# Optimization experiments

Measured on AMD Instinct MI355X. Metric: run time of the kernel, lower is better.

The kernel has to match this reference:

```python
import jax, jax.numpy as jnp
import numpy as np

B, T, I, H = 4096, 256, 6, 64


def _gru_layer(x, W_ih, W_hh, b_ih, b_hh):
    # x: [B,T,Din]; W_ih: [3H,Din]; W_hh: [3H,H]
    xg = jnp.einsum('btd,gd->btg', x, W_ih) + b_ih  # [B,T,3H] input projections
    xg = jnp.transpose(xg, (1, 0, 2))               # [T,B,3H] for scan
    h0 = jnp.zeros((x.shape[0], H), dtype=x.dtype)

    def step(h, xg_t):
        hg = h @ W_hh.T + b_hh                      # [B,3H]
        xr, xz, xn = jnp.split(xg_t, 3, axis=-1)
        hr, hz, hn = jnp.split(hg, 3, axis=-1)
        r = jax.nn.sigmoid(xr + hr)
        z = jax.nn.sigmoid(xz + hz)
        n = jnp.tanh(xn + r * hn)
        h_new = (1.0 - z) * n + z * h
        return h_new, h_new

    _, hs = jax.lax.scan(step, h0, xg)              # hs: [T,B,H]
    return jnp.transpose(hs, (1, 0, 2))             # [B,T,H]


def setup_inputs() -> dict:
    key = jax.random.key(0)
    ks = jax.random.split(key, 11)
    s_i0 = 1.0 / np.sqrt(H)
    u = lambda k, shape: jax.random.uniform(k, shape, jnp.float32, -s_i0, s_i0)
    return {
        'x': jax.random.normal(ks[0], (B, T, I), dtype=jnp.float32),
        'W_ih0': u(ks[1], (3 * H, I)),
        'W_hh0': u(ks[2], (3 * H, H)),
        'b_ih0': u(ks[3], (3 * H,)),
        'b_hh0': u(ks[4], (3 * H,)),
        'W_ih1': u(ks[5], (3 * H, H)),
        'W_hh1': u(ks[6], (3 * H, H)),
        'b_ih1': u(ks[7], (3 * H,)),
        'b_hh1': u(ks[8], (3 * H,)),
        'W_fc': u(ks[9], (1, H)),
        'b_fc': u(ks[10], (1,)),
    }


def reference(x, W_ih0, W_hh0, b_ih0, b_hh0, W_ih1, W_hh1, b_ih1, b_hh1, W_fc, b_fc):
    h1 = _gru_layer(x, W_ih0, W_hh0, b_ih0, b_hh0)   # [B,T,H]
    h2 = _gru_layer(h1, W_ih1, W_hh1, b_ih1, b_hh1)  # [B,T,H]
    last = h2[:, -1, :]                              # [B,H] (dropout is identity in eval)
    out = last @ W_fc.T + b_fc                       # [B,1]
    return out[:, 0]                                 # squeeze(-1) -> [B]
```

## Files before the change

### kernel.cpp

```cpp
#include <hip/hip_runtime.h>
#include <stdint.h>

#define TT 256
#define II 6
#define HH 64
#define MB 16

typedef __attribute__((ext_vector_type(8))) _Float16 half8;
typedef __attribute__((ext_vector_type(4))) float f32x4;

#define K_LOG2E  1.44269504f
#define K_2LOG2E 2.88539008f

static __device__ __forceinline__ uint32_t pkh(float a, float b){
    uint16_t ha = __builtin_bit_cast(uint16_t, (_Float16)a);
    uint16_t hb = __builtin_bit_cast(uint16_t, (_Float16)b);
    return (uint32_t)ha | ((uint32_t)hb << 16);
}
static __device__ __forceinline__ half8 mkh8(uint32_t a, uint32_t b, uint32_t c, uint32_t d){
    union { uint32_t u[4]; half8 v; } x;
    x.u[0]=a; x.u[1]=b; x.u[2]=c; x.u[3]=d;
    return x.v;
}
static __device__ __forceinline__ half8 ldq(const uint32_t* p){
    union { uint4 q; half8 v; } x;
    x.q = *(const uint4*)p;
    return x.v;
}

#define MF(C, A, B) C = __builtin_amdgcn_mfma_f32_16x16x32_f16(A, B, C, 0, 0, 0)

static __device__ __forceinline__ uint2 gates(const f32x4& Cr, const f32x4& Cz,
                                              const f32x4& Cxn, const f32x4& Chn,
                                              f32x4& hp)
{
    float hn[4];
    #pragma unroll
    for (int q = 0; q < 4; ++q){
        float er = __builtin_amdgcn_exp2f(-Cr[q]);
        float ez = __builtin_amdgcn_exp2f(-Cz[q]);
        float pa = 1.0f + er, pb = 1.0f + ez;
        float u  = __builtin_amdgcn_rcpf(pa * pb);
        float rg = u * pb;
        float zg = u * pa;
        float v  = Cxn[q] + rg * Chn[q];
        float e  = __builtin_amdgcn_exp2f(-v);
        float ng = (1.0f - e) * __builtin_amdgcn_rcpf(1.0f + e);
        float h2 = ng + zg * (hp[q] - ng);
        hp[q] = h2;
        hn[q] = h2;
    }
    return make_uint2(pkh(hn[0], hn[1]), pkh(hn[2], hn[3]));
}

__global__ __launch_bounds__(512, 2)
void gru2_v6(const float* __restrict__ x,
             const float* __restrict__ Wih0, const float* __restrict__ Whh0,
             const float* __restrict__ bih0, const float* __restrict__ bhh0,
             const float* __restrict__ Wih1, const float* __restrict__ Whh1,
             const float* __restrict__ bih1, const float* __restrict__ bhh1,
             const float* __restrict__ Wfc,  const float* __restrict__ bfc,
             float* __restrict__ out)
{
    __shared__ uint2    xtA[TT][16];
    __shared__ uint32_t xtB[TT][16];
    __shared__ uint32_t h0buf[2][16][36];
    __shared__ uint32_t h1buf[2][16][36];
    __shared__ float    fcpart[256];

    const int tid  = threadIdx.x;
    const int lane = tid & 63;
    const int wg   = tid >> 6;
    const int isL1 = (wg >= 4);
    const int w    = wg & 3;
    const int c    = lane >> 4;
    const int r16  = lane & 15;
    const int b0   = blockIdx.x * MB;

    for (int e = tid; e < TT * 16; e += 512){
        const int t = e & 255, b = e >> 8;
        const int bi_ = (b + t) & 15;
        const float* xp = x + ((size_t)(b0 + b) * TT + t) * II;
        float2 a  = *(const float2*)(xp + 0);
        float2 bb = *(const float2*)(xp + 2);
        float2 cc = *(const float2*)(xp + 4);
        xtA[t][bi_] = make_uint2(pkh(a.x, a.y), pkh(bb.x, bb.y));
        xtB[t][bi_] = pkh(cc.x, cc.y);
    }
    for (int i = tid; i < 2 * 16 * 36; i += 512){
        (&h0buf[0][0][0])[i] = 0u;
        (&h1buf[0][0][0])[i] = 0u;
    }

    const float gsc[3] = { K_LOG2E, K_LOG2E, K_2LOG2E };
    half8 AW[6][2];
    {
        const float* M0 = isL1 ? Wih1 : Whh0;
        #pragma unroll
        for (int m = 0; m < 6; ++m){
            if (m >= 3 && !isL1) continue;
            const float* Wb = (m < 3) ? M0 : Whh1;
            const float s = gsc[m % 3];
            const float* rowp = Wb + (size_t)((m % 3) * 64 + w * 16 + r16) * HH;
            #pragma unroll
            for (int cw = 0; cw < 2; ++cw){
                const float* pp = rowp + cw * 32 + c * 8;
                AW[m][cw] = mkh8(pkh(s*pp[0], s*pp[1]), pkh(s*pp[2], s*pp[3]),
                                 pkh(s*pp[4], s*pp[5]), pkh(s*pp[6], s*pp[7]));
            }
        }
    }

    half8 Ax[3];
    #pragma unroll
    for (int g = 0; g < 3; ++g){
        if (c == 0){
            const float s = gsc[g];
            const float* rowp = Wih0 + (size_t)(g * 64 + w * 16 + r16) * II;
            Ax[g] = mkh8(pkh(s*rowp[0], s*rowp[1]), pkh(s*rowp[2], s*rowp[3]),
                         pkh(s*rowp[4], s*rowp[5]), 0u);
        } else {
            Ax[g] = mkh8(0u, 0u, 0u, 0u);
        }
    }

    const float* bi = isL1 ? bih1 : bih0;
    const float* bh = isL1 ? bhh1 : bhh0;
    const int rq0 = w * 16 + c * 4;
    f32x4 Br, Bz, Bxn, Bhn;
    #pragma unroll
    for (int q = 0; q < 4; ++q){
        Br[q]  = K_LOG2E  * (bi[      rq0 + q] + bh[      rq0 + q]);
        Bz[q]  = K_LOG2E  * (bi[ 64 + rq0 + q] + bh[ 64 + rq0 + q]);
        Bxn[q] = K_2LOG2E *  bi[128 + rq0 + q];
        Bhn[q] = K_2LOG2E *  bh[128 + rq0 + q];
    }

    f32x4 hp = {0.f, 0.f, 0.f, 0.f};

    const uint32_t* rd0p[2] = { &h0buf[0][r16][4*c], &h0buf[1][r16][4*c] };
    const uint32_t* rd1p[2] = { &h1buf[0][r16][4*c], &h1buf[1][r16][4*c] };
    uint2* wr0p[2] = { (uint2*)&h0buf[0][r16][8*w + 2*c], (uint2*)&h0buf[1][r16][8*w + 2*c] };
    uint2* wr1p[2] = { (uint2*)&h1buf[0][r16][8*w + 2*c], (uint2*)&h1buf[1][r16][8*w + 2*c] };

    __syncthreads();

#define TICK(P, D0, D1, TK) do {                                               \
    if (!isL1) { if (D0) {                                                     \
        const int xi = ((r16 + (TK)) & 15);                                    \
        uint2 xa = xtA[(TK)][xi];                                              \
        uint32_t xb = xtB[(TK)][xi];                                           \
        half8 XB = mkh8(xa.x, xa.y, xb, 0u);                                   \
        f32x4 Cr = Br, Cz = Bz, Cxn = Bxn, Chn = Bhn;                          \
        __builtin_amdgcn_s_setprio(1);                                         \
        MF(Cr,  Ax[0], XB);  MF(Cz,  Ax[1], XB);  MF(Cxn, Ax[2], XB);          \
        { half8 HB = ldq(rd0p[P]);                                             \
          MF(Cr, AW[0][0], HB); MF(Cz, AW[1][0], HB); MF(Chn, AW[2][0], HB); } \
        { half8 HB = ldq(rd0p[P] + 16);                                        \
          MF(Cr, AW[0][1], HB); MF(Cz, AW[1][1], HB); MF(Chn, AW[2][1], HB); } \
        __builtin_amdgcn_s_setprio(0);                                         \
        uint2 d = gates(Cr, Cz, Cxn, Chn, hp);                                 \
        *wr0p[(P) ^ 1] = d;                                                    \
    } } else { if (D1) {                                                       \
        f32x4 Cr = Br, Cz = Bz, Cxn = Bxn, Chn = Bhn;                          \
        __builtin_amdgcn_s_setprio(1);                                         \
        { half8 HB = ldq(rd0p[P]);                                             \
          MF(Cr, AW[0][0], HB); MF(Cz, AW[1][0], HB); MF(Cxn, AW[2][0], HB); } \
        { half8 HB = ldq(rd0p[P] + 16);                                        \
          MF(Cr, AW[0][1], HB); MF(Cz, AW[1][1], HB); MF(Cxn, AW[2][1], HB); } \
        { half8 HB = ldq(rd1p[P]);                                             \
          MF(Cr, AW[3][0], HB); MF(Cz, AW[4][0], HB); MF(Chn, AW[5][0], HB); } \
        { half8 HB = ldq(rd1p[P] + 16);                                        \
          MF(Cr, AW[3][1], HB); MF(Cz, AW[4][1], HB); MF(Chn, AW[5][1], HB); } \
        __builtin_amdgcn_s_setprio(0);                                         \
        uint2 d = gates(Cr, Cz, Cxn, Chn, hp);                                 \
        *wr1p[(P) ^ 1] = d;                                                    \
    } }                                                                        \
} while (0)

    TICK(0, true, false, 0);
    __syncthreads();
    #pragma unroll 1
    for (int tk = 1; tk < 255; tk += 2){
        TICK(1, true, true, tk);
        __syncthreads();
        TICK(0, true, true, tk + 1);
        __syncthreads();
    }
    TICK(1, true, true, 255);
    __syncthreads();
    TICK(0, false, true, 256);

#undef TICK

    if (isL1){
        float4 wf = *(const float4*)(Wfc + w * 16 + c * 4);
        fcpart[(w * 4 + c) * 16 + r16] =
            hp[0] * wf.x + hp[1] * wf.y + hp[2] * wf.z + hp[3] * wf.w;
    }
    __syncthreads();
    if (tid < MB){
        float s = bfc[0];
        #pragma unroll
        for (int u = 0; u < 16; ++u) s += fcpart[u * 16 + tid];
        out[b0 + tid] = s;
    }
}

extern "C" void kernel_launch(void* const* d_in, const int* in_sizes, int n_in,
                              void* d_out, int out_size, void* d_ws, size_t ws_size,
                              hipStream_t stream)
{
    const float* x    = (const float*)d_in[0];
    const float* Wih0 = (const float*)d_in[1];
    const float* Whh0 = (const float*)d_in[2];
    const float* bih0 = (const float*)d_in[3];
    const float* bhh0 = (const float*)d_in[4];
    const float* Wih1 = (const float*)d_in[5];
    const float* Whh1 = (const float*)d_in[6];
    const float* bih1 = (const float*)d_in[7];
    const float* bhh1 = (const float*)d_in[8];
    const float* Wfc  = (const float*)d_in[9];
    const float* bfc  = (const float*)d_in[10];
    float* out = (float*)d_out;

    dim3 grid(4096 / MB), block(512);
    gru2_v6<<<grid, block, 0, stream>>>(x, Wih0, Whh0, bih0, bhh0,
                                        Wih1, Whh1, bih1, bhh1,
                                        Wfc, bfc, out);
}
```

Baseline: 143.1 us.

## Stream x from global per step and precompute next input projection off critical path

```diff
diff --git a/kernel.cpp b/kernel.cpp
--- a/kernel.cpp
+++ b/kernel.cpp
@@ -16,6 +16,9 @@
     uint16_t ha = __builtin_bit_cast(uint16_t, (_Float16)a);
     uint16_t hb = __builtin_bit_cast(uint16_t, (_Float16)b);
     return (uint32_t)ha | ((uint32_t)hb << 16);
+}
+static __device__ __forceinline__ uint32_t pkrtz(float a, float b){
+    return __builtin_bit_cast(uint32_t, __builtin_amdgcn_cvt_pkrtz(a, b));
 }
 static __device__ __forceinline__ half8 mkh8(uint32_t a, uint32_t b, uint32_t c, uint32_t d){
     union { uint32_t u[4]; half8 v; } x;
@@ -47,14 +50,13 @@
         float e  = __builtin_amdgcn_exp2f(-v);
         float ng = (1.0f - e) * __builtin_amdgcn_rcpf(1.0f + e);
         float h2 = ng + zg * (hp[q] - ng);
-        hp[q] = h2;
-        hn[q] = h2;
-    }
-    return make_uint2(pkh(hn[0], hn[1]), pkh(hn[2], hn[3]));
+        hp[q] = h2; hn[q] = h2;
+    }
+    return make_uint2(pkrtz(hn[0], hn[1]), pkrtz(hn[2], hn[3]));
 }
 
 __global__ __launch_bounds__(512, 2)
-void gru2_v6(const float* __restrict__ x,
+void gru2_v7(const float* __restrict__ x,
              const float* __restrict__ Wih0, const float* __restrict__ Whh0,
              const float* __restrict__ bih0, const float* __restrict__ bhh0,
              const float* __restrict__ Wih1, const float* __restrict__ Whh1,
@@ -62,11 +64,9 @@
              const float* __restrict__ Wfc,  const float* __restrict__ bfc,
              float* __restrict__ out)
 {
-    __shared__ uint2    xtA[TT][16];
-    __shared__ uint32_t xtB[TT][16];
-    __shared__ uint32_t h0buf[2][16][36];
-    __shared__ uint32_t h1buf[2][16][36];
-    __shared__ float    fcpart[256];
+    __shared__ uint32_t h0buf[2][MB][36];
+    __shared__ uint32_t h1buf[2][MB][36];
+    __shared__ float    fcpart[16][MB];
 
     const int tid  = threadIdx.x;
     const int lane = tid & 63;
@@ -77,17 +77,7 @@
     const int r16  = lane & 15;
     const int b0   = blockIdx.x * MB;
 
-    for (int e = tid; e < TT * 16; e += 512){
-        const int t = e & 255, b = e >> 8;
-        const int bi_ = (b + t) & 15;
-        const float* xp = x + ((size_t)(b0 + b) * TT + t) * II;
-        float2 a  = *(const float2*)(xp + 0);
-        float2 bb = *(const float2*)(xp + 2);
-        float2 cc = *(const float2*)(xp + 4);
-        xtA[t][bi_] = make_uint2(pkh(a.x, a.y), pkh(bb.x, bb.y));
-        xtB[t][bi_] = pkh(cc.x, cc.y);
-    }
-    for (int i = tid; i < 2 * 16 * 36; i += 512){
+    for (int i = tid; i < 2 * MB * 36; i += 512){
         (&h0buf[0][0][0])[i] = 0u;
         (&h1buf[0][0][0])[i] = 0u;
     }
@@ -110,11 +100,10 @@
             }
         }
     }
-
     half8 Ax[3];
     #pragma unroll
     for (int g = 0; g < 3; ++g){
-        if (c == 0){
+        if (c == 0 && !isL1){
             const float s = gsc[g];
             const float* rowp = Wih0 + (size_t)(g * 64 + w * 16 + r16) * II;
             Ax[g] = mkh8(pkh(s*rowp[0], s*rowp[1]), pkh(s*rowp[2], s*rowp[3]),
@@ -138,71 +127,97 @@
 
     f32x4 hp = {0.f, 0.f, 0.f, 0.f};
 
-    const uint32_t* rd0p[2] = { &h0buf[0][r16][4*c], &h0buf[1][r16][4*c] };
-    const uint32_t* rd1p[2] = { &h1buf[0][r16][4*c], &h1buf[1][r16][4*c] };
-    uint2* wr0p[2] = { (uint2*)&h0buf[0][r16][8*w + 2*c], (uint2*)&h0buf[1][r16][8*w + 2*c] };
-    uint2* wr1p[2] = { (uint2*)&h1buf[0][r16][8*w + 2*c], (uint2*)&h1buf[1][r16][8*w + 2*c] };
-
-    __syncthreads();
-
-#define TICK(P, D0, D1, TK) do {                                               \
-    if (!isL1) { if (D0) {                                                     \
-        const int xi = ((r16 + (TK)) & 15);                                    \
-        uint2 xa = xtA[(TK)][xi];                                              \
-        uint32_t xb = xtB[(TK)][xi];                                           \
-        half8 XB = mkh8(xa.x, xa.y, xb, 0u);                                   \
-        f32x4 Cr = Br, Cz = Bz, Cxn = Bxn, Chn = Bhn;                          \
-        __builtin_amdgcn_s_setprio(1);                                         \
-        MF(Cr,  Ax[0], XB);  MF(Cz,  Ax[1], XB);  MF(Cxn, Ax[2], XB);          \
-        { half8 HB = ldq(rd0p[P]);                                             \
-          MF(Cr, AW[0][0], HB); MF(Cz, AW[1][0], HB); MF(Chn, AW[2][0], HB); } \
-        { half8 HB = ldq(rd0p[P] + 16);                                        \
-          MF(Cr, AW[0][1], HB); MF(Cz, AW[1][1], HB); MF(Chn, AW[2][1], HB); } \
-        __builtin_amdgcn_s_setprio(0);                                         \
-        uint2 d = gates(Cr, Cz, Cxn, Chn, hp);                                 \
-        *wr0p[(P) ^ 1] = d;                                                    \
-    } } else { if (D1) {                                                       \
-        f32x4 Cr = Br, Cz = Bz, Cxn = Bxn, Chn = Bhn;                          \
-        __builtin_amdgcn_s_setprio(1);                                         \
-        { half8 HB = ldq(rd0p[P]);                                             \
-          MF(Cr, AW[0][0], HB); MF(Cz, AW[1][0], HB); MF(Cxn, AW[2][0], HB); } \
-        { half8 HB = ldq(rd0p[P] + 16);                                        \
-          MF(Cr, AW[0][1], HB); MF(Cz, AW[1][1], HB); MF(Cxn, AW[2][1], HB); } \
-        { half8 HB = ldq(rd1p[P]);                                             \
-          MF(Cr, AW[3][0], HB); MF(Cz, AW[4][0], HB); MF(Chn, AW[5][0], HB); } \
-        { half8 HB = ldq(rd1p[P] + 16);                                        \
-          MF(Cr, AW[3][1], HB); MF(Cz, AW[4][1], HB); MF(Chn, AW[5][1], HB); } \
-        __builtin_amdgcn_s_setprio(0);                                         \
-        uint2 d = gates(Cr, Cz, Cxn, Chn, hp);                                 \
-        *wr1p[(P) ^ 1] = d;                                                    \
-    } }                                                                        \
-} while (0)
-
-    TICK(0, true, false, 0);
+    const uint32_t* rd0[2] = { &h0buf[0][r16][4*c], &h0buf[1][r16][4*c] };
+    const uint32_t* rd1[2] = { &h1buf[0][r16][4*c], &h1buf[1][r16][4*c] };
+    uint2* wr0[2] = { (uint2*)&h0buf[0][r16][8*w + 2*c], (uint2*)&h0buf[1][r16][8*w + 2*c] };
+    uint2* wr1[2] = { (uint2*)&h1buf[0][r16][8*w + 2*c], (uint2*)&h1buf[1][r16][8*w + 2*c] };
+
+    f32x4 CrS[2], CzS[2], CxnS[2], ChnS[2];
+
+    const float* xq = nullptr;
+    float2 x0v, x1v, x2v;
+    if (!isL1){
+        xq = x + (size_t)(b0 + r16) * (TT * II);
+        float2 a  = *(const float2*)(xq + 0);
+        float2 bb = *(const float2*)(xq + 2);
+        float2 cc = *(const float2*)(xq + 4);
+        half8 XB = mkh8(pkrtz(a.x, a.y), pkrtz(bb.x, bb.y), pkrtz(cc.x, cc.y), 0u);
+        CrS[0]=Br; CzS[0]=Bz; CxnS[0]=Bxn; ChnS[0]=Bhn;
+        MF(CrS[0], Ax[0], XB); MF(CzS[0], Ax[1], XB); MF(CxnS[0], Ax[2], XB);
+        xq += II;
+        x0v = *(const float2*)(xq + 0);
+        x1v = *(const float2*)(xq + 2);
+        x2v = *(const float2*)(xq + 4);
+    } else {
+        CrS[1]=Br; CzS[1]=Bz; CxnS[1]=Bxn; ChnS[1]=Bhn;
+    }
+    __syncthreads();
+
+#define L0TICK(P, TK) do {                                                          \
+    half8 H0 = ldq(rd0[P]);                                                         \
+    half8 H1 = ldq(rd0[P] + 16);                                                    \
+    __builtin_amdgcn_s_setprio(1);                                                  \
+    MF(CrS[P],  AW[0][0], H0); MF(CzS[P],  AW[1][0], H0); MF(ChnS[P], AW[2][0], H0);\
+    MF(CrS[P],  AW[0][1], H1); MF(CzS[P],  AW[1][1], H1); MF(ChnS[P], AW[2][1], H1);\
+    __builtin_amdgcn_s_setprio(0);                                                  \
+    uint2 d = gates(CrS[P], CzS[P], CxnS[P], ChnS[P], hp);                          \
+    *wr0[(P) ^ 1] = d;                                                              \
+    if ((TK) + 1 < TT){           \
+        half8 XB = mkh8(pkrtz(x0v.x, x0v.y), pkrtz(x1v.x, x1v.y),                   \
+                        pkrtz(x2v.x, x2v.y), 0u);                                   \
+        CrS[(P)^1]=Br; CzS[(P)^1]=Bz; CxnS[(P)^1]=Bxn; ChnS[(P)^1]=Bhn;             \
+        MF(CrS[(P)^1], Ax[0], XB); MF(CzS[(P)^1], Ax[1], XB); MF(CxnS[(P)^1], Ax[2], XB); \
+        if ((TK) + 2 < TT){                                                         \
+            xq += II;                                                               \
+            x0v = *(const float2*)(xq + 0);                                         \
+            x1v = *(const float2*)(xq + 2);                                         \
+            x2v = *(const float2*)(xq + 4);                                         \
+        }                                                                           \
+    }                                                                               \
+} while(0)
+
+#define L1TICK(P) do {                                                              \
+    half8 G0 = ldq(rd0[P]);                                                         \
+    half8 G1 = ldq(rd0[P] + 16);                                                    \
+    half8 H0 = ldq(rd1[P]);                                                         \
+    half8 H1 = ldq(rd1[P] + 16);                                                    \
+    __builtin_amdgcn_s_setprio(1);                                                  \
+    MF(CrS[P], AW[0][0], G0); MF(CzS[P], AW[1][0], G0); MF(CxnS[P], AW[2][0], G0);  \
+    MF(CrS[P], AW[0][1], G1); MF(CzS[P], AW[1][1], G1); MF(CxnS[P], AW[2][1], G1);  \
+    MF(CrS[P], AW[3][0], H0); MF(CzS[P], AW[4][0], H0); MF(ChnS[P], AW[5][0], H0);  \
+    MF(CrS[P], AW[3][1], H1); MF(CzS[P], AW[4][1], H1); MF(ChnS[P], AW[5][1], H1);  \
+    __builtin_amdgcn_s_setprio(0);                                                  \
+    uint2 d = gates(CrS[P], CzS[P], CxnS[P], ChnS[P], hp);                          \
+    *wr1[(P) ^ 1] = d;                                                              \
+    CrS[(P)^1]=Br; CzS[(P)^1]=Bz; CxnS[(P)^1]=Bxn; ChnS[(P)^1]=Bhn;                 \
+} while(0)
+
+    if (!isL1) L0TICK(0, 0);
     __syncthreads();
     #pragma unroll 1
     for (int tk = 1; tk < 255; tk += 2){
-        TICK(1, true, true, tk);
+        if (!isL1) L0TICK(1, tk); else L1TICK(1);
         __syncthreads();
-        TICK(0, true, true, tk + 1);
+        if (!isL1) L0TICK(0, tk + 1); else L1TICK(0);
         __syncthreads();
     }
-    TICK(1, true, true, 255);
-    __syncthreads();
-    TICK(0, false, true, 256);
-
-#undef TICK
+    if (!isL1) L0TICK(1, 255); else L1TICK(1);
+    __syncthreads();
+    if (isL1) L1TICK(0);
+
+#undef L0TICK
+#undef L1TICK
 
     if (isL1){
         float4 wf = *(const float4*)(Wfc + w * 16 + c * 4);
-        fcpart[(w * 4 + c) * 16 + r16] =
+        fcpart[w * 4 + c][r16] =
             hp[0] * wf.x + hp[1] * wf.y + hp[2] * wf.z + hp[3] * wf.w;
     }
     __syncthreads();
     if (tid < MB){
         float s = bfc[0];
         #pragma unroll
-        for (int u = 0; u < 16; ++u) s += fcpart[u * 16 + tid];
+        for (int k = 0; k < 16; ++k) s += fcpart[k][tid];
         out[b0 + tid] = s;
     }
 }
@@ -225,7 +240,7 @@
     float* out = (float*)d_out;
 
     dim3 grid(4096 / MB), block(512);
-    gru2_v6<<<grid, block, 0, stream>>>(x, Wih0, Whh0, bih0, bhh0,
+    gru2_v7<<<grid, block, 0, stream>>>(x, Wih0, Whh0, bih0, bhh0,
                                         Wih1, Whh1, bih1, bhh1,
                                         Wfc, bfc, out);
 }
```

Measured after the change: 142.3 us. About the same (-0.5%).
